# Optimization experiments

Hardware: AMD Instinct MI355X
Metric: run time of the kernel (lower is better)

## Reference

```python
import jax, jax.numpy as jnp
import numpy as np

NH = 16      # num_heads
EPS = 1e-6   # RMSNorm eps


def rmsnorm(x, w):
    return x * jax.lax.rsqrt(jnp.mean(x * x, axis=-1, keepdims=True) + EPS) * w


def rotate_half(x):
    x1, x2 = jnp.split(x, 2, axis=-1)
    return jnp.concatenate([-x2, x1], axis=-1)


def apply_rope(x, cos, sin):
    # x: [B,H,N,hd]; cos/sin: [N,hd]
    return x * cos + rotate_half(x) * sin


def attention(x, qkv_w, qkv_b, qn_w, kn_w, proj_w, proj_b, cos, sin):
    B, N, C = x.shape
    hd = C // NH
    qkv = (x @ qkv_w.T + qkv_b).reshape(B, N, 3, NH, hd).transpose(2, 0, 3, 1, 4)
    q, k, v = qkv[0], qkv[1], qkv[2]            # [B,H,N,hd]
    q = apply_rope(rmsnorm(q, qn_w), cos, sin)
    k = apply_rope(rmsnorm(k, kn_w), cos, sin)
    scores = jnp.einsum('bhqd,bhkd->bhqk', q, k) / jnp.sqrt(jnp.float32(hd))
    attn = jax.nn.softmax(scores, axis=-1)
    out = jnp.einsum('bhqk,bhkd->bhqd', attn, v)
    out = out.transpose(0, 2, 1, 3).reshape(B, N, C)
    return out @ proj_w.T + proj_b


def jit_block(x, c, cos_s, sin_s, cos_t, sin_t,
              norm1_w, norm2_w, norm3_w,
              qkv_s_w, qkv_s_b, qn_s_w, kn_s_w, proj_s_w, proj_s_b,
              qkv_t_w, qkv_t_b, qn_t_w, kn_t_w, proj_t_w, proj_t_b,
              w12_w, w12_b, w3_w, w3_b, ada_w, ada_b):
    B, T, L, D = x.shape
    mods = (jax.nn.silu(c) @ ada_w.T + ada_b).reshape(B, 9, D)
    sh_s, sc_s, g_s = mods[:, 0], mods[:, 1], mods[:, 2]
    sh_t, sc_t, g_t = mods[:, 3], mods[:, 4], mods[:, 5]
    sh_m, sc_m, g_m = mods[:, 6], mods[:, 7], mods[:, 8]

    # spatial attention over L, batched over B*T
    xs = x.reshape(B * T, L, D)
    sh = jnp.repeat(sh_s, T, axis=0)
    sc = jnp.repeat(sc_s, T, axis=0)
    g = jnp.repeat(g_s, T, axis=0)
    xs_n = rmsnorm(xs, norm1_w) * (1 + sc[:, None, :]) + sh[:, None, :]
    xs = xs + g[:, None, :] * attention(xs_n, qkv_s_w, qkv_s_b, qn_s_w, kn_s_w,
                                        proj_s_w, proj_s_b, cos_s, sin_s)
    x = xs.reshape(B, T, L, D)

    # temporal attention over T, batched over B*L
    xt = x.transpose(0, 2, 1, 3).reshape(B * L, T, D)
    sh = jnp.repeat(sh_t, L, axis=0)
    sc = jnp.repeat(sc_t, L, axis=0)
    g = jnp.repeat(g_t, L, axis=0)
    xt_n = rmsnorm(xt, norm2_w) * (1 + sc[:, None, :]) + sh[:, None, :]
    xt = xt + g[:, None, :] * attention(xt_n, qkv_t_w, qkv_t_b, qn_t_w, kn_t_w,
                                        proj_t_w, proj_t_b, cos_t, sin_t)
    x = xt.reshape(B, L, T, D).transpose(0, 2, 1, 3)

    # SwiGLU FFN with adaLN modulation + gate
    x_n = rmsnorm(x, norm3_w) * (1 + sc_m[:, None, None, :]) + sh_m[:, None, None, :]
    h12 = x_n @ w12_w.T + w12_b
    h1, h2 = jnp.split(h12, 2, axis=-1)
    mlp_out = (jax.nn.silu(h1) * h2) @ w3_w.T + w3_b
    return x + g_m[:, None, None, :] * mlp_out


def _rope_tables(n, hd):
    inv = 1.0 / (10000.0 ** (np.arange(0, hd, 2, dtype=np.float64) / hd))
    ang = np.arange(n, dtype=np.float64)[:, None] * inv[None, :]
    cos = np.concatenate([np.cos(ang), np.cos(ang)], -1).astype(np.float32)
    sin = np.concatenate([np.sin(ang), np.sin(ang)], -1).astype(np.float32)
    return jnp.asarray(cos), jnp.asarray(sin)


def setup_inputs() -> dict:
    key = jax.random.key(0)
    B, T, L, D = 2, 16, 256, 1024
    HD = D // NH
    HFF = int(int(D * 4.0) * 2 / 3)  # 2730
    ks = jax.random.split(key, 16)
    s = 0.02
    cos_s, sin_s = _rope_tables(L, HD)
    cos_t, sin_t = _rope_tables(T, HD)
    return {
        'x': jax.random.normal(ks[0], (B, T, L, D), jnp.float32),
        'c': jax.random.normal(ks[1], (B, D), jnp.float32),
        'cos_s': cos_s, 'sin_s': sin_s, 'cos_t': cos_t, 'sin_t': sin_t,
        'norm1_w': jnp.ones((D,), jnp.float32),
        'norm2_w': jnp.ones((D,), jnp.float32),
        'norm3_w': jnp.ones((D,), jnp.float32),
        'qkv_s_w': jax.random.normal(ks[2], (3 * D, D), jnp.float32) * s,
        'qkv_s_b': jnp.zeros((3 * D,), jnp.float32),
        'qn_s_w': jnp.ones((HD,), jnp.float32),
        'kn_s_w': jnp.ones((HD,), jnp.float32),
        'proj_s_w': jax.random.normal(ks[3], (D, D), jnp.float32) * s,
        'proj_s_b': jnp.zeros((D,), jnp.float32),
        'qkv_t_w': jax.random.normal(ks[4], (3 * D, D), jnp.float32) * s,
        'qkv_t_b': jnp.zeros((3 * D,), jnp.float32),
        'qn_t_w': jnp.ones((HD,), jnp.float32),
        'kn_t_w': jnp.ones((HD,), jnp.float32),
        'proj_t_w': jax.random.normal(ks[5], (D, D), jnp.float32) * s,
        'proj_t_b': jnp.zeros((D,), jnp.float32),
        'w12_w': jax.random.normal(ks[6], (2 * HFF, D), jnp.float32) * s,
        'w12_b': jnp.zeros((2 * HFF,), jnp.float32),
        'w3_w': jax.random.normal(ks[7], (D, HFF), jnp.float32) * s,
        'w3_b': jnp.zeros((D,), jnp.float32),
        'ada_w': jax.random.normal(ks[8], (9 * D, D), jnp.float32) * s,
        'ada_b': jnp.zeros((9 * D,), jnp.float32),
    }


def reference(x, c, cos_s, sin_s, cos_t, sin_t,
              norm1_w, norm2_w, norm3_w,
              qkv_s_w, qkv_s_b, qn_s_w, kn_s_w, proj_s_w, proj_s_b,
              qkv_t_w, qkv_t_b, qn_t_w, kn_t_w, proj_t_w, proj_t_b,
              w12_w, w12_b, w3_w, w3_b, ada_w, ada_b):
    return jit_block(x, c, cos_s, sin_s, cos_t, sin_t,
                     norm1_w, norm2_w, norm3_w,
                     qkv_s_w, qkv_s_b, qn_s_w, kn_s_w, proj_s_w, proj_s_b,
                     qkv_t_w, qkv_t_b, qn_t_w, kn_t_w, proj_t_w, proj_t_b,
                     w12_w, w12_b, w3_w, w3_b, ada_w, ada_b)
```

## Files before the change

### kernel.cpp

```cpp
#include <hip/hip_runtime.h>
#include <cstdint>
#include <cstddef>

typedef unsigned short u16;
typedef __attribute__((ext_vector_type(8))) short short8;
typedef __attribute__((ext_vector_type(4))) float f32x4;

__device__ __forceinline__ float bf2f(u16 u) {
  union { uint32_t u; float f; } x; x.u = ((uint32_t)u) << 16; return x.f;
}
__device__ __forceinline__ u16 f2bf(float f) {
  union { float f; uint32_t u; } x; x.f = f;
  uint32_t r = x.u + 0x7FFFu + ((x.u >> 16) & 1u);
  return (u16)(r >> 16);
}
__device__ __forceinline__ float silu_f(float x) { return x / (1.f + __expf(-x)); }

__device__ __forceinline__ void glds16(const u16* g, u16* l) {
  __builtin_amdgcn_global_load_lds(
      (const __attribute__((address_space(1))) void*)g,
      (__attribute__((address_space(3))) void*)l, 16, 0, 0);
}

#define MFMA16 __builtin_amdgcn_mfma_f32_16x16x32_bf16

__device__ __forceinline__ void wg_barrier() {
  asm volatile("" ::: "memory");
  __builtin_amdgcn_s_barrier();
  asm volatile("" ::: "memory");
}

__global__ void cvt2_kernel(const float* __restrict__ in0, u16* __restrict__ out0, int n0,
                            const float* __restrict__ in1, u16* __restrict__ out1, int n1) {
  int i = (blockIdx.x * 256 + threadIdx.x) * 4;
  const float* in; u16* out;
  if (i < n0) { in = in0 + i; out = out0 + i; }
  else { i -= n0; if (i >= n1) return; in = in1 + i; out = out1 + i; }
  float4 v = *(const float4*)in;
  ushort4 o; o.x = f2bf(v.x); o.y = f2bf(v.y); o.z = f2bf(v.z); o.w = f2bf(v.w);
  *(ushort4*)out = o;
}

__global__ void cvt3_kernel(const float* __restrict__ w12, u16* __restrict__ W1, u16* __restrict__ W2,
                            const float* __restrict__ w3, u16* __restrict__ W3) {
  int i = blockIdx.x * 256 + threadIdx.x;
  const int n1 = 2816 * 1024;
  const int n3 = 1024 * 2816;
  if (i < n1) {
    int r = i >> 10, c = i & 1023;
    W1[i] = f2bf(r < 2730 ? w12[(size_t)r * 1024 + c] : 0.f);
  } else if (i < 2 * n1) {
    int j = i - n1; int r = j >> 10, c = j & 1023;
    W2[j] = f2bf(r < 2730 ? w12[(size_t)(r + 2730) * 1024 + c] : 0.f);
  } else {
    int j = i - 2 * n1; if (j >= n3) return;
    int r = j / 2816, c = j - r * 2816;
    W3[j] = f2bf(c < 2730 ? w3[(size_t)r * 2730 + c] : 0.f);
  }
}

__global__ void mods_kernel(const float* __restrict__ c, const float* __restrict__ ada_w,
                            const float* __restrict__ ada_b, float* __restrict__ mods) {
  int j = blockIdx.x * 4 + (threadIdx.x >> 6);
  int lane = threadIdx.x & 63;
  float a0 = 0.f, a1 = 0.f;
  for (int k = lane; k < 1024; k += 64) {
    float w = ada_w[(size_t)j * 1024 + k];
    a0 += silu_f(c[k]) * w;
    a1 += silu_f(c[1024 + k]) * w;
  }
  #pragma unroll
  for (int off = 32; off > 0; off >>= 1) { a0 += __shfl_down(a0, off); a1 += __shfl_down(a1, off); }
  if (lane == 0) {
    float bb = ada_b[j];
    mods[j] = a0 + bb;
    mods[9216 + j] = a1 + bb;
  }
}

__global__ __launch_bounds__(256) void norm_mod_kernel(
    const float* __restrict__ X, u16* __restrict__ Y,
    const float* __restrict__ nw, const float* __restrict__ mods,
    int sh_idx, int transpose) {
  int row = blockIdx.x;
  int b = row >> 12;
  int in_row;
  if (transpose) { int rem = row & 4095; int l = rem >> 4, t = rem & 15; in_row = (b << 12) + (t << 8) + l; }
  else in_row = row;
  int tid = threadIdx.x;
  float4 v = ((const float4*)(X + (size_t)in_row * 1024))[tid];
  float ss = v.x * v.x + v.y * v.y + v.z * v.z + v.w * v.w;
  #pragma unroll
  for (int off = 32; off > 0; off >>= 1) ss += __shfl_down(ss, off);
  __shared__ float red[4];
  if ((tid & 63) == 0) red[tid >> 6] = ss;
  __syncthreads();
  float rms = rsqrtf((red[0] + red[1] + red[2] + red[3]) * (1.f / 1024.f) + 1e-6f);
  const float* mb = mods + (size_t)b * 9216 + (size_t)sh_idx * 1024;
  float4 sh = ((const float4*)mb)[tid];
  float4 sc = ((const float4*)(mb + 1024))[tid];
  float4 w  = ((const float4*)nw)[tid];
  ushort4 o;
  o.x = f2bf(v.x * rms * w.x * (1.f + sc.x) + sh.x);
  o.y = f2bf(v.y * rms * w.y * (1.f + sc.y) + sh.y);
  o.z = f2bf(v.z * rms * w.z * (1.f + sc.z) + sh.z);
  o.w = f2bf(v.w * rms * w.w * (1.f + sc.w) + sh.w);
  ((ushort4*)(Y + (size_t)row * 1024))[tid] = o;
}

#define CHK2(b, s) (((b) * 4 + (s)) << 13)
#define CHK3(b, s) (((b) * 3 + (s)) << 13)

__device__ __forceinline__ void stage_half(const u16* __restrict__ gp, int ldk,
                                           int row_base, int k0,
                                           u16* Sbase, int slot_u16,
                                           int wid, int srow, int scol) {
  #pragma unroll
  for (int c = 0; c < 2; c++) {
    int row = c * 64 + wid * 8 + srow;
    glds16(gp + (size_t)(row_base + row) * ldk + (k0 + scol),
           Sbase + slot_u16 + c * 4096 + wid * 512);
  }
}

template<int MODE>
__global__ __launch_bounds__(512, 2) void gemm256_n128(
    const u16* __restrict__ A, const u16* __restrict__ W,
    const float* __restrict__ bias, void* __restrict__ Cv,
    int K, int ldc,
    const float* __restrict__ base, const float* __restrict__ mods, int gidx) {
  __shared__ u16 S[49152];
  const int tid = threadIdx.x, wid = tid >> 6, lane = tid & 63;
  const int wm = wid >> 1, wn = wid & 1;
  const int quad = lane >> 4, r = lane & 15;
  const int bid = blockIdx.x, xcd = bid & 7, l = bid >> 3;
  const int mt = (xcd << 2) | (l & 3), nt = l >> 2;
  const int m0 = mt * 256, n0 = nt * 128;

  const int srow = lane >> 3;
  const int scol = ((lane & 7) ^ srow) << 3;
  const int kx0 = (quad * 8) ^ ((r & 7) << 3);
  const int kx1 = (32 + quad * 8) ^ ((r & 7) << 3);
  const int aslot = wm >> 1;
  const int arow = ((wm & 1) * 64 + r) * 64;
  const int brow = (wn * 64 + r) * 64;

  f32x4 zero = {0.f, 0.f, 0.f, 0.f};
  f32x4 acc[4][4];
  #pragma unroll
  for (int i = 0; i < 4; i++)
    #pragma unroll
    for (int j = 0; j < 4; j++) acc[i][j] = zero;
  short8 fAa[4][2], fBa[4][2], fAb[4][2], fBb[4][2];

  const int nk = K >> 6;

  const u16* gA0c0 = A + (size_t)(m0 +       wid * 8 + srow) * K + scol + 128;
  const u16* gA0c1 = A + (size_t)(m0 +  64 + wid * 8 + srow) * K + scol + 128;
  const u16* gA1c0 = A + (size_t)(m0 + 128 + wid * 8 + srow) * K + scol + 128;
  const u16* gA1c1 = A + (size_t)(m0 + 192 + wid * 8 + srow) * K + scol + 128;
  const u16* gBc0  = W + (size_t)(n0 +       wid * 8 + srow) * K + scol + 128;
  const u16* gBc1  = W + (size_t)(n0 +  64 + wid * 8 + srow) * K + scol + 128;

  stage_half(A, K, m0,       0, S, CHK3(0,0), wid, srow, scol);
  stage_half(A, K, m0 + 128, 0, S, CHK3(0,1), wid, srow, scol);
  stage_half(W, K, n0,       0, S, CHK3(0,2), wid, srow, scol);
  stage_half(A, K, m0,       64, S, CHK3(1,0), wid, srow, scol);
  stage_half(A, K, m0 + 128, 64, S, CHK3(1,1), wid, srow, scol);
  stage_half(W, K, n0,       64, S, CHK3(1,2), wid, srow, scol);
  asm volatile("s_waitcnt vmcnt(0)" ::: "memory");
  __builtin_amdgcn_s_barrier();

  {
    const u16* cA = S + CHK3(0, aslot);
    const u16* cB = S + CHK3(0, 2);
    #pragma unroll
    for (int f = 0; f < 4; f++) {
      fAa[f][0] = *(const short8*)(cA + arow + f * 1024 + kx0);
      fAa[f][1] = *(const short8*)(cA + arow + f * 1024 + kx1);
    }
    #pragma unroll
    for (int j = 0; j < 4; j++) {
      fBa[j][0] = *(const short8*)(cB + brow + j * 1024 + kx0);
      fBa[j][1] = *(const short8*)(cB + brow + j * 1024 + kx1);
    }
  }
  asm volatile("s_waitcnt lgkmcnt(0)" ::: "memory");
  __builtin_amdgcn_s_barrier();

  for (int u2 = 0; u2 < nk; u2 += 2) {
    const int s2a = (u2 + 2 < nk);
    if (s2a) {
      u16* Sb = S + wid * 512;
      glds16(gA0c0, Sb);          glds16(gA0c1, Sb + 4096);
      glds16(gA1c0, Sb + 8192);   glds16(gA1c1, Sb + 12288);
      glds16(gBc0,  Sb + 16384);  glds16(gBc1,  Sb + 20480);
      gA0c0 += 64; gA0c1 += 64; gA1c0 += 64; gA1c1 += 64; gBc0 += 64; gBc1 += 64;
    }
    {
      const u16* cA = S + CHK3(1, aslot);
      const u16* cB = S + CHK3(1, 2);
      #pragma unroll
      for (int f = 0; f < 4; f++) {
        fAb[f][0] = *(const short8*)(cA + arow + f * 1024 + kx0);
        fAb[f][1] = *(const short8*)(cA + arow + f * 1024 + kx1);
      }
      #pragma unroll
      for (int j = 0; j < 4; j++) {
        fBb[j][0] = *(const short8*)(cB + brow + j * 1024 + kx0);
        fBb[j][1] = *(const short8*)(cB + brow + j * 1024 + kx1);
      }
    }
    __builtin_amdgcn_s_setprio(1);
    #pragma unroll
    for (int f = 0; f < 4; f++)
      #pragma unroll
      for (int j = 0; j < 4; j++) {
        acc[f][j] = MFMA16(fAa[f][0], fBa[j][0], acc[f][j], 0, 0, 0);
        acc[f][j] = MFMA16(fAa[f][1], fBa[j][1], acc[f][j], 0, 0, 0);
      }
    __builtin_amdgcn_s_setprio(0);
    asm volatile("s_waitcnt lgkmcnt(0)" ::: "memory");
    if (s2a) asm volatile("s_waitcnt vmcnt(0)" ::: "memory");
    __builtin_amdgcn_s_barrier();

    const int s2b = (u2 + 3 < nk);
    if (s2b) {
      u16* Sb = S + 24576 + wid * 512;
      glds16(gA0c0, Sb);          glds16(gA0c1, Sb + 4096);
      glds16(gA1c0, Sb + 8192);   glds16(gA1c1, Sb + 12288);
      glds16(gBc0,  Sb + 16384);  glds16(gBc1,  Sb + 20480);
      gA0c0 += 64; gA0c1 += 64; gA1c0 += 64; gA1c1 += 64; gBc0 += 64; gBc1 += 64;
    }
    if (s2a) {
      const u16* cA = S + CHK3(0, aslot);
      const u16* cB = S + CHK3(0, 2);
      #pragma unroll
      for (int f = 0; f < 4; f++) {
        fAa[f][0] = *(const short8*)(cA + arow + f * 1024 + kx0);
        fAa[f][1] = *(const short8*)(cA + arow + f * 1024 + kx1);
      }
      #pragma unroll
      for (int j = 0; j < 4; j++) {
        fBa[j][0] = *(const short8*)(cB + brow + j * 1024 + kx0);
        fBa[j][1] = *(const short8*)(cB + brow + j * 1024 + kx1);
      }
    }
    __builtin_amdgcn_s_setprio(1);
    #pragma unroll
    for (int f = 0; f < 4; f++)
      #pragma unroll
      for (int j = 0; j < 4; j++) {
        acc[f][j] = MFMA16(fAb[f][0], fBb[j][0], acc[f][j], 0, 0, 0);
        acc[f][j] = MFMA16(fAb[f][1], fBb[j][1], acc[f][j], 0, 0, 0);
      }
    __builtin_amdgcn_s_setprio(0);
    if (s2a) asm volatile("s_waitcnt lgkmcnt(0)" ::: "memory");
    if (s2b) asm volatile("s_waitcnt vmcnt(0)" ::: "memory");
    __builtin_amdgcn_s_barrier();
  }

  float* Cf = (float*)Cv;
  u16* Ch = (u16*)Cv;
  #pragma unroll
  for (int f = 0; f < 4; f++) {
    int row = m0 + wm * 64 + f * 16 + quad * 4;
    #pragma unroll
    for (int j = 0; j < 4; j++) {
      int col = n0 + wn * 64 + j * 16 + r;
      float bv = bias[col];
      #pragma unroll
      for (int rr = 0; rr < 4; rr++) {
        int ri = row + rr;
        float vv = acc[f][j][rr] + bv;
        if (MODE == 0) {
          Cf[(size_t)ri * ldc + col] = vv;
        } else if (MODE == 1) {
          Ch[(size_t)ri * ldc + col] = f2bf(vv);
        } else {
          int ro = ri;
          if (MODE == 3) { int rem = ri & 4095; ro = (ri & ~4095) + ((rem & 15) << 8) + (rem >> 4); }
          int b = ri >> 12;
          float g = mods[(size_t)b * 9216 + (size_t)gidx * 1024 + col];
          Cf[(size_t)ro * 1024 + col] = base[(size_t)ro * 1024 + col] + g * vv;
        }
      }
    }
  }
}

__global__ __launch_bounds__(512, 2) void gemm256_w12(
    const u16* __restrict__ A, const u16* __restrict__ W1, const u16* __restrict__ W2,
    const float* __restrict__ bias, u16* __restrict__ Hb) {
  __shared__ u16 S[65536];
  const int tid = threadIdx.x, wid = tid >> 6, lane = tid & 63;
  const int wm = wid >> 2, wn = wid & 3;
  const int quad = lane >> 4, r = lane & 15;
  const int bid = blockIdx.x, xcd = bid & 7, l = bid >> 3;
  const int mt = (xcd << 2) | (l & 3), nt = l >> 2;
  const int m0 = mt * 256, n0 = nt * 128;

  const int srow = lane >> 3;
  const int scol = ((lane & 7) ^ srow) << 3;
  const int kx0 = (quad * 8) ^ ((r & 7) << 3);
  const int kx1 = (32 + quad * 8) ^ ((r & 7) << 3);
  const int arow = (wm * 64 + r) * 64;
  const int brow = (wn * 32 + r) * 64;
  const int K = 1024, nk = 16;

  f32x4 zero = {0.f, 0.f, 0.f, 0.f};
  f32x4 acc1[8][2], acc2[8][2];
  #pragma unroll
  for (int i = 0; i < 8; i++)
    #pragma unroll
    for (int j = 0; j < 2; j++) { acc1[i][j] = zero; acc2[i][j] = zero; }
  short8 fA[4][2], fW1[2][2], fW2[2][2];

  const u16* gA0c0 = A  + (size_t)(m0 +       wid * 8 + srow) * K + scol + 128;
  const u16* gA0c1 = A  + (size_t)(m0 +  64 + wid * 8 + srow) * K + scol + 128;
  const u16* gA1c0 = A  + (size_t)(m0 + 128 + wid * 8 + srow) * K + scol + 128;
  const u16* gA1c1 = A  + (size_t)(m0 + 192 + wid * 8 + srow) * K + scol + 128;
  const u16* gW1c0 = W1 + (size_t)(n0 +       wid * 8 + srow) * K + scol + 128;
  const u16* gW1c1 = W1 + (size_t)(n0 +  64 + wid * 8 + srow) * K + scol + 128;
  const u16* gW2c0 = W2 + (size_t)(n0 +       wid * 8 + srow) * K + scol + 128;
  const u16* gW2c1 = W2 + (size_t)(n0 +  64 + wid * 8 + srow) * K + scol + 128;

  stage_half(A,  K, m0,       0, S, CHK2(0,0), wid, srow, scol);
  stage_half(W1, K, n0,       0, S, CHK2(0,2), wid, srow, scol);
  stage_half(W2, K, n0,       0, S, CHK2(0,3), wid, srow, scol);
  stage_half(A,  K, m0 + 128, 0, S, CHK2(0,1), wid, srow, scol);
  stage_half(A,  K, m0,      64, S, CHK2(1,0), wid, srow, scol);
  stage_half(W1, K, n0,      64, S, CHK2(1,2), wid, srow, scol);
  stage_half(W2, K, n0,      64, S, CHK2(1,3), wid, srow, scol);
  stage_half(A,  K, m0 + 128,64, S, CHK2(1,1), wid, srow, scol);
  asm volatile("s_waitcnt vmcnt(8)" ::: "memory");
  __builtin_amdgcn_s_barrier();

  for (int u = 0; u < nk; ++u) {
    const int cur = u & 1;
    const int s1 = (u + 1 < nk), s2 = (u + 2 < nk);
    const u16* cA0 = S + CHK2(cur, 0);
    const u16* cA1 = S + CHK2(cur, 1);
    const u16* cW1 = S + CHK2(cur, 2);
    const u16* cW2 = S + CHK2(cur, 3);
    u16* Sb = S + cur * 32768 + wid * 512;

    #pragma unroll
    for (int f = 0; f < 4; f++) {
      fA[f][0] = *(const short8*)(cA0 + arow + f * 1024 + kx0);
      fA[f][1] = *(const short8*)(cA0 + arow + f * 1024 + kx1);
    }
    #pragma unroll
    for (int j = 0; j < 2; j++) {
      fW1[j][0] = *(const short8*)(cW1 + brow + j * 1024 + kx0);
      fW1[j][1] = *(const short8*)(cW1 + brow + j * 1024 + kx1);
      fW2[j][0] = *(const short8*)(cW2 + brow + j * 1024 + kx0);
      fW2[j][1] = *(const short8*)(cW2 + brow + j * 1024 + kx1);
    }
    wg_barrier();

    if (s2) {
      glds16(gA0c0, Sb);          glds16(gA0c1, Sb + 4096);
      glds16(gW1c0, Sb + 16384);  glds16(gW1c1, Sb + 20480);
      glds16(gW2c0, Sb + 24576);  glds16(gW2c1, Sb + 28672);
    }
    __builtin_amdgcn_s_setprio(1);
    #pragma unroll
    for (int f = 0; f < 4; f++)
      #pragma unroll
      for (int j = 0; j < 2; j++) {
        acc1[f][j] = MFMA16(fA[f][0], fW1[j][0], acc1[f][j], 0, 0, 0);
        acc1[f][j] = MFMA16(fA[f][1], fW1[j][1], acc1[f][j], 0, 0, 0);
        acc2[f][j] = MFMA16(fA[f][0], fW2[j][0], acc2[f][j], 0, 0, 0);
        acc2[f][j] = MFMA16(fA[f][1], fW2[j][1], acc2[f][j], 0, 0, 0);
      }
    __builtin_amdgcn_s_setprio(0);
    #pragma unroll
    for (int f = 0; f < 4; f++) {
      fA[f][0] = *(const short8*)(cA1 + arow + f * 1024 + kx0);
      fA[f][1] = *(const short8*)(cA1 + arow + f * 1024 + kx1);
    }
    wg_barrier();

    if (s2) { glds16(gA1c0, Sb + 8192); glds16(gA1c1, Sb + 12288); }
    gA0c0 += 64; gA0c1 += 64; gA1c0 += 64; gA1c1 += 64;
    gW1c0 += 64; gW1c1 += 64; gW2c0 += 64; gW2c1 += 64;
    __builtin_amdgcn_s_setprio(1);
    #pragma unroll
    for (int f = 0; f < 4; f++)
      #pragma unroll
      for (int j = 0; j < 2; j++) {
        acc1[4 + f][j] = MFMA16(fA[f][0], fW1[j][0], acc1[4 + f][j], 0, 0, 0);
        acc1[4 + f][j] = MFMA16(fA[f][1], fW1[j][1], acc1[4 + f][j], 0, 0, 0);
        acc2[4 + f][j] = MFMA16(fA[f][0], fW2[j][0], acc2[4 + f][j], 0, 0, 0);
        acc2[4 + f][j] = MFMA16(fA[f][1], fW2[j][1], acc2[4 + f][j], 0, 0, 0);
      }
    __builtin_amdgcn_s_setprio(0);
    if (s2)      asm volatile("s_waitcnt vmcnt(8)" ::: "memory");
    else if (s1) asm volatile("s_waitcnt vmcnt(0)" ::: "memory");
    wg_barrier();
  }

  #pragma unroll
  for (int f = 0; f < 8; f++) {
    int row = m0 + (f >> 2) * 128 + wm * 64 + (f & 3) * 16 + quad * 4;
    #pragma unroll
    for (int j = 0; j < 2; j++) {
      int col = n0 + wn * 32 + j * 16 + r;
      float b1 = (col < 2730) ? bias[col] : 0.f;
      float b2 = (col < 2730) ? bias[2730 + col] : 0.f;
      #pragma unroll
      for (int rr = 0; rr < 4; rr++) {
        float h1 = acc1[f][j][rr] + b1;
        float h2 = acc2[f][j][rr] + b2;
        Hb[(size_t)(row + rr) * 2816 + col] = f2bf(silu_f(h1) * h2);
      }
    }
  }
}

#define KSS 72
#define VSS 264
#define PSS 40
__global__ __launch_bounds__(512) void attn_s_mfma(
    const u16* __restrict__ QKV,
    const float* __restrict__ qn_w, const float* __restrict__ kn_w,
    const float* __restrict__ cosT, const float* __restrict__ sinT,
    u16* __restrict__ AO) {
  __shared__ u16 Ks[256 * KSS];
  __shared__ u16 Vt[64 * VSS];
  __shared__ u16 Pl[8 * 32 * PSS];
  int pair = blockIdx.x;
  int s = pair >> 4, h = pair & 15;
  int tid = threadIdx.x, wid = tid >> 6, lane = tid & 63;
  int quad = lane >> 4, r = lane & 15;

  if (tid < 256) {
    int j = tid;
    size_t rowb = ((size_t)(s * 256 + j)) * 3072 + (size_t)h * 64;
    const short8* kr = (const short8*)(QKV + rowb + 1024);
    float xk[64]; float ssq = 0.f;
    #pragma unroll
    for (int cg = 0; cg < 8; cg++) {
      short8 kk = kr[cg];
      #pragma unroll
      for (int e = 0; e < 8; e++) { float v = bf2f((u16)kk[e]); xk[cg * 8 + e] = v; ssq += v * v; }
    }
    float rms = rsqrtf(ssq * (1.f / 64.f) + 1e-6f);
    short8 kq[8];
    #pragma unroll
    for (int d = 0; d < 32; d++) {
      float a = xk[d] * rms * kn_w[d];
      float b2 = xk[d + 32] * rms * kn_w[d + 32];
      u16 o0 = f2bf(a * cosT[j * 64 + d] - b2 * sinT[j * 64 + d]);
      u16 o1 = f2bf(b2 * cosT[j * 64 + 32 + d] + a * sinT[j * 64 + 32 + d]);
      kq[d >> 3][d & 7] = (short)o0;
      kq[(d + 32) >> 3][d & 7] = (short)o1;
    }
    #pragma unroll
    for (int cg = 0; cg < 8; cg++) *(short8*)(Ks + j * KSS + cg * 8) = kq[cg];
  } else {
    int j = tid - 256;
    size_t rowb = ((size_t)(s * 256 + j)) * 3072 + (size_t)h * 64;
    const short8* vr = (const short8*)(QKV + rowb + 2048);
    #pragma unroll
    for (int cg = 0; cg < 8; cg++) {
      short8 vv = vr[cg];
      #pragma unroll
      for (int e = 0; e < 8; e++) Vt[(cg * 8 + e) * VSS + j] = (u16)vv[e];
    }
  }

  int qbase = wid * 32;
  short8 qa[2][2];
  float lrow[2][4];
  {
    float qv[2][2][8];
    float ssq[2] = {0.f, 0.f};
    #pragma unroll
    for (int i = 0; i < 2; i++) {
      int grow = s * 256 + qbase + i * 16 + r;
      #pragma unroll
      for (int kk = 0; kk < 2; kk++) {
        short8 qraw = *(const short8*)(QKV + (size_t)grow * 3072 + h * 64 + kk * 32 + quad * 8);
        #pragma unroll
        for (int e = 0; e < 8; e++) { float v = bf2f((u16)qraw[e]); qv[i][kk][e] = v; ssq[i] += v * v; }
      }
    }
    #pragma unroll
    for (int i = 0; i < 2; i++) {
      float sv = ssq[i];
      sv += __shfl_xor(sv, 16);
      sv += __shfl_xor(sv, 32);
      float rms = rsqrtf(sv * (1.f / 64.f) + 1e-6f);
      int qrow = qbase + i * 16 + r;
      #pragma unroll
      for (int e = 0; e < 8; e++) {
        int d0 = quad * 8 + e;
        float a = qv[i][0][e] * rms * qn_w[d0];
        float b2 = qv[i][1][e] * rms * qn_w[d0 + 32];
        qa[i][0][e] = (short)f2bf(a * cosT[qrow * 64 + d0] - b2 * sinT[qrow * 64 + d0]);
        qa[i][1][e] = (short)f2bf(b2 * cosT[qrow * 64 + 32 + d0] + a * sinT[qrow * 64 + 32 + d0]);
      }
    }
  }
  __syncthreads();

  f32x4 zero = {0.f, 0.f, 0.f, 0.f};
  f32x4 acc[2][16];
  #pragma unroll
  for (int i = 0; i < 2; i++)
    #pragma unroll
    for (int j = 0; j < 16; j++) acc[i][j] = zero;
  #pragma unroll
  for (int kk = 0; kk < 2; kk++) {
    #pragma unroll
    for (int j = 0; j < 16; j++) {
      short8 bfr = *(const short8*)(Ks + (j * 16 + r) * KSS + kk * 32 + quad * 8);
      acc[0][j] = MFMA16(qa[0][kk], bfr, acc[0][j], 0, 0, 0);
      acc[1][j] = MFMA16(qa[1][kk], bfr, acc[1][j], 0, 0, 0);
    }
  }

  #pragma unroll
  for (int i = 0; i < 2; i++) {
    #pragma unroll
    for (int rr = 0; rr < 4; rr++) {
      float mx = acc[i][0][rr];
      #pragma unroll
      for (int j = 1; j < 16; j++) mx = fmaxf(mx, acc[i][j][rr]);
      #pragma unroll
      for (int msk = 1; msk < 16; msk <<= 1) mx = fmaxf(mx, __shfl_xor(mx, msk));
      float ls = 0.f;
      #pragma unroll
      for (int j = 0; j < 16; j++) { float p = __expf((acc[i][j][rr] - mx) * 0.125f); acc[i][j][rr] = p; ls += p; }
      #pragma unroll
      for (int msk = 1; msk < 16; msk <<= 1) ls += __shfl_xor(ls, msk);
      lrow[i][rr] = ls;
    }
  }

  f32x4 oacc[2][4];
  #pragma unroll
  for (int i = 0; i < 2; i++)
    #pragma unroll
    for (int j = 0; j < 4; j++) oacc[i][j] = zero;
  u16* plw = Pl + wid * 32 * PSS;
  #pragma unroll
  for (int kk = 0; kk < 8; kk++) {
    #pragma unroll
    for (int i = 0; i < 2; i++)
      #pragma unroll
      for (int jj = 0; jj < 2; jj++) {
        int j = kk * 2 + jj;
        #pragma unroll
        for (int rr = 0; rr < 4; rr++)
          plw[(i * 16 + quad * 4 + rr) * PSS + jj * 16 + r] = f2bf(acc[i][j][rr]);
      }
    short8 pa0 = *(const short8*)(plw + r * PSS + quad * 8);
    short8 pa1 = *(const short8*)(plw + (16 + r) * PSS + quad * 8);
    #pragma unroll
    for (int j4 = 0; j4 < 4; j4++) {
      short8 vfr = *(const short8*)(Vt + (j4 * 16 + r) * VSS + kk * 32 + quad * 8);
      oacc[0][j4] = MFMA16(pa0, vfr, oacc[0][j4], 0, 0, 0);
      oacc[1][j4] = MFMA16(pa1, vfr, oacc[1][j4], 0, 0, 0);
    }
  }

  #pragma unroll
  for (int i = 0; i < 2; i++) {
    #pragma unroll
    for (int rr = 0; rr < 4; rr++) {
      float inv = 1.f / lrow[i][rr];
      int row = s * 256 + qbase + i * 16 + quad * 4 + rr;
      #pragma unroll
      for (int j4 = 0; j4 < 4; j4++)
        AO[(size_t)row * 1024 + h * 64 + j4 * 16 + r] = f2bf(oacc[i][j4][rr] * inv);
    }
  }
}

__global__ __launch_bounds__(256) void attn_t_kernel(
    const u16* __restrict__ QKV,
    const float* __restrict__ qn_w, const float* __restrict__ kn_w,
    const float* __restrict__ cosT, const float* __restrict__ sinT,
    u16* __restrict__ AO) {
  __shared__ u16 kb[256 * 64];
  __shared__ u16 vb[256 * 64];
  int bl = blockIdx.x;
  int tid = threadIdx.x;
  int h = tid >> 4, t = tid & 15;
  size_t rowbase = ((size_t)(bl * 16 + t)) * 3072;
  int slot = h * 16 + t;
  {
    const u16* kr = QKV + rowbase + 1024 + h * 64;
    float xk[64]; float ss = 0.f;
    #pragma unroll
    for (int d = 0; d < 64; d++) { xk[d] = bf2f(kr[d]); ss += xk[d] * xk[d]; }
    float rms = rsqrtf(ss * (1.f / 64.f) + 1e-6f);
    #pragma unroll
    for (int d = 0; d < 64; d++) xk[d] *= rms * kn_w[d];
    #pragma unroll
    for (int d = 0; d < 32; d++) {
      float a = xk[d], bb = xk[d + 32];
      kb[slot * 64 + d]      = f2bf(a * cosT[t * 64 + d]       - bb * sinT[t * 64 + d]);
      kb[slot * 64 + 32 + d] = f2bf(bb * cosT[t * 64 + 32 + d] + a * sinT[t * 64 + 32 + d]);
    }
    const u16* vr = QKV + rowbase + 2048 + h * 64;
    #pragma unroll
    for (int d = 0; d < 64; d++) vb[slot * 64 + d] = vr[d];
  }
  float q[64];
  {
    const u16* qr = QKV + rowbase + h * 64;
    float ss = 0.f;
    #pragma unroll
    for (int d = 0; d < 64; d++) { q[d] = bf2f(qr[d]); ss += q[d] * q[d]; }
    float rms = rsqrtf(ss * (1.f / 64.f) + 1e-6f);
    #pragma unroll
    for (int d = 0; d < 64; d++) q[d] *= rms * qn_w[d];
    #pragma unroll
    for (int d = 0; d < 32; d++) {
      float a = q[d], bb = q[d + 32];
      q[d]      = a * cosT[t * 64 + d]       - bb * sinT[t * 64 + d];
      q[d + 32] = bb * cosT[t * 64 + 32 + d] + a * sinT[t * 64 + 32 + d];
    }
  }
  __syncthreads();
  float scv[16]; float mx = -1e30f;
  #pragma unroll
  for (int j = 0; j < 16; j++) {
    float sc = 0.f;
    const short8* krow = (const short8*)(kb + (h * 16 + j) * 64);
    #pragma unroll
    for (int vv = 0; vv < 8; vv++) {
      short8 kk = krow[vv];
      #pragma unroll
      for (int e = 0; e < 8; e++) sc += q[vv * 8 + e] * bf2f((u16)kk[e]);
    }
    scv[j] = sc * 0.125f;
    mx = fmaxf(mx, scv[j]);
  }
  float ssum = 0.f;
  #pragma unroll
  for (int j = 0; j < 16; j++) { scv[j] = __expf(scv[j] - mx); ssum += scv[j]; }
  float inv = 1.f / ssum;
  float o[64];
  #pragma unroll
  for (int d = 0; d < 64; d++) o[d] = 0.f;
  #pragma unroll
  for (int j = 0; j < 16; j++) {
    const short8* vrow = (const short8*)(vb + (h * 16 + j) * 64);
    #pragma unroll
    for (int vv = 0; vv < 8; vv++) {
      short8 vk = vrow[vv];
      #pragma unroll
      for (int e = 0; e < 8; e++) o[vv * 8 + e] += scv[j] * bf2f((u16)vk[e]);
    }
  }
  u16* op = AO + ((size_t)(bl * 16 + t)) * 1024 + h * 64;
  #pragma unroll
  for (int d = 0; d < 64; d++) op[d] = f2bf(o[d] * inv);
}

extern "C" void kernel_launch(void* const* d_in, const int* in_sizes, int n_in,
                              void* d_out, int out_size, void* d_ws, size_t ws_size,
                              hipStream_t stream) {
  const float* x        = (const float*)d_in[0];
  const float* c        = (const float*)d_in[1];
  const float* cos_s    = (const float*)d_in[2];
  const float* sin_s    = (const float*)d_in[3];
  const float* cos_t    = (const float*)d_in[4];
  const float* sin_t    = (const float*)d_in[5];
  const float* norm1w   = (const float*)d_in[6];
  const float* norm2w   = (const float*)d_in[7];
  const float* norm3w   = (const float*)d_in[8];
  const float* qkv_s_w  = (const float*)d_in[9];
  const float* qkv_s_b  = (const float*)d_in[10];
  const float* qn_s_w   = (const float*)d_in[11];
  const float* kn_s_w   = (const float*)d_in[12];
  const float* proj_s_w = (const float*)d_in[13];
  const float* proj_s_b = (const float*)d_in[14];
  const float* qkv_t_w  = (const float*)d_in[15];
  const float* qkv_t_b  = (const float*)d_in[16];
  const float* qn_t_w   = (const float*)d_in[17];
  const float* kn_t_w   = (const float*)d_in[18];
  const float* proj_t_w = (const float*)d_in[19];
  const float* proj_t_b = (const float*)d_in[20];
  const float* w12_w    = (const float*)d_in[21];
  const float* w12_b    = (const float*)d_in[22];
  const float* w3_w     = (const float*)d_in[23];
  const float* w3_b     = (const float*)d_in[24];
  const float* ada_w    = (const float*)d_in[25];
  const float* ada_b    = (const float*)d_in[26];
  float* out = (float*)d_out;

  char* wsp = (char*)d_ws;
  size_t off = 0;
  auto alloc = [&](size_t bytes) { size_t p = off; off += (bytes + 255) & ~(size_t)255; return p; };
  float* modsb = (float*)(wsp + alloc(2 * 9216 * 4));
  u16*   BIG   = (u16*)  (wsp + alloc((size_t)8192 * 3072 * 2));
  char*  XnP   = (char*) (wsp + alloc((size_t)8192 * 1024 * 4));
  u16*   AO    = (u16*)  (wsp + alloc((size_t)8192 * 1024 * 2));
  u16*   Wq    = (u16*)  (wsp + alloc((size_t)3072 * 1024 * 2));
  u16*   Wp    = (u16*)  (wsp + alloc((size_t)2816 * 1024 * 2));
  u16*   W3b   = (u16*)  (wsp + alloc((size_t)1024 * 2816 * 2));
  u16* W1p = Wq;
  u16* W2p = Wp;
  u16* Xn  = (u16*)XnP;
  float* Xcur = out;

  dim3 blk(256);
  dim3 blk512(512);
  mods_kernel<<<2304, blk, 0, stream>>>(c, ada_w, ada_b, modsb);

  {
    int n0 = 3072 * 1024, n1 = 1024 * 1024;
    cvt2_kernel<<<(n0 + n1) / 1024, blk, 0, stream>>>(qkv_s_w, Wq, n0, proj_s_w, Wp, n1);
  }
  norm_mod_kernel<<<8192, blk, 0, stream>>>(x, Xn, norm1w, modsb, 0, 0);
  gemm256_n128<1><<<dim3(32 * 24), blk512, 0, stream>>>(Xn, Wq, qkv_s_b, BIG, 1024, 3072, nullptr, nullptr, 0);
  attn_s_mfma<<<dim3(512), blk512, 0, stream>>>(BIG, qn_s_w, kn_s_w, cos_s, sin_s, AO);
  gemm256_n128<2><<<dim3(32 * 8), blk512, 0, stream>>>(AO, Wp, proj_s_b, Xcur, 1024, 1024, x, modsb, 2);

  {
    int n0 = 3072 * 1024, n1 = 1024 * 1024;
    cvt2_kernel<<<(n0 + n1) / 1024, blk, 0, stream>>>(qkv_t_w, Wq, n0, proj_t_w, Wp, n1);
  }
  norm_mod_kernel<<<8192, blk, 0, stream>>>(Xcur, Xn, norm2w, modsb, 3, 1);
  gemm256_n128<1><<<dim3(32 * 24), blk512, 0, stream>>>(Xn, Wq, qkv_t_b, BIG, 1024, 3072, nullptr, nullptr, 0);
  attn_t_kernel<<<512, blk, 0, stream>>>(BIG, qn_t_w, kn_t_w, cos_t, sin_t, AO);
  gemm256_n128<3><<<dim3(32 * 8), blk512, 0, stream>>>(AO, Wp, proj_t_b, Xcur, 1024, 1024, Xcur, modsb, 5);

  {
    int tot = 2 * 2816 * 1024 + 1024 * 2816;
    cvt3_kernel<<<(tot + 255) / 256, blk, 0, stream>>>(w12_w, W1p, W2p, w3_w, W3b);
  }
  norm_mod_kernel<<<8192, blk, 0, stream>>>(Xcur, Xn, norm3w, modsb, 6, 0);
  gemm256_w12<<<dim3(32 * 22), blk512, 0, stream>>>(Xn, W1p, W2p, w12_b, BIG);
  gemm256_n128<2><<<dim3(32 * 8), blk512, 0, stream>>>(BIG, W3b, w3_b, out, 2816, 1024, Xcur, modsb, 8);
}
```

Before: 641.3 us.

## Shrink SwiGLU GEMM M-tile to 128 with register-prefetched LDS double buffer

The fused W1/W2 SwiGLU GEMM now uses 128x128 output tiles instead of 256x128, doubling the grid to 1408 blocks and halving the accumulator registers and shared memory. The main loop is restructured into a two-stage ping-pong. Fragments for the next K-step are read from LDS into a second register set while MFMAs run on the current set, and global-to-LDS loads are issued one step ahead. This aims to improve occupancy, tail balance and latency hiding, at the cost of lower operand reuse per block and full vmcnt(0) waits each step.

```diff
diff --git a/kernel.cpp b/kernel.cpp
--- a/kernel.cpp
+++ b/kernel.cpp
@@ -108,7 +108,6 @@
   ((ushort4*)(Y + (size_t)row * 1024))[tid] = o;
 }
 
-#define CHK2(b, s) (((b) * 4 + (s)) << 13)
 #define CHK3(b, s) (((b) * 3 + (s)) << 13)
 
 __device__ __forceinline__ void stage_half(const u16* __restrict__ gp, int ldk,
@@ -289,16 +288,16 @@
   }
 }
 
-__global__ __launch_bounds__(512, 2) void gemm256_w12(
+__global__ __launch_bounds__(512, 2) void gemm128_w12(
     const u16* __restrict__ A, const u16* __restrict__ W1, const u16* __restrict__ W2,
     const float* __restrict__ bias, u16* __restrict__ Hb) {
-  __shared__ u16 S[65536];
+  __shared__ u16 S[49152];
   const int tid = threadIdx.x, wid = tid >> 6, lane = tid & 63;
   const int wm = wid >> 2, wn = wid & 3;
   const int quad = lane >> 4, r = lane & 15;
   const int bid = blockIdx.x, xcd = bid & 7, l = bid >> 3;
-  const int mt = (xcd << 2) | (l & 3), nt = l >> 2;
-  const int m0 = mt * 256, n0 = nt * 128;
+  const int mt = (xcd << 3) | (l & 7), nt = l >> 3;
+  const int m0 = mt * 128, n0 = nt * 128;
 
   const int srow = lane >> 3;
   const int scol = ((lane & 7) ^ srow) << 3;
@@ -309,101 +308,135 @@
   const int K = 1024, nk = 16;
 
   f32x4 zero = {0.f, 0.f, 0.f, 0.f};
-  f32x4 acc1[8][2], acc2[8][2];
-  #pragma unroll
-  for (int i = 0; i < 8; i++)
+  f32x4 acc1[4][2], acc2[4][2];
+  #pragma unroll
+  for (int i = 0; i < 4; i++)
     #pragma unroll
     for (int j = 0; j < 2; j++) { acc1[i][j] = zero; acc2[i][j] = zero; }
-  short8 fA[4][2], fW1[2][2], fW2[2][2];
-
-  const u16* gA0c0 = A  + (size_t)(m0 +       wid * 8 + srow) * K + scol + 128;
-  const u16* gA0c1 = A  + (size_t)(m0 +  64 + wid * 8 + srow) * K + scol + 128;
-  const u16* gA1c0 = A  + (size_t)(m0 + 128 + wid * 8 + srow) * K + scol + 128;
-  const u16* gA1c1 = A  + (size_t)(m0 + 192 + wid * 8 + srow) * K + scol + 128;
-  const u16* gW1c0 = W1 + (size_t)(n0 +       wid * 8 + srow) * K + scol + 128;
-  const u16* gW1c1 = W1 + (size_t)(n0 +  64 + wid * 8 + srow) * K + scol + 128;
-  const u16* gW2c0 = W2 + (size_t)(n0 +       wid * 8 + srow) * K + scol + 128;
-  const u16* gW2c1 = W2 + (size_t)(n0 +  64 + wid * 8 + srow) * K + scol + 128;
-
-  stage_half(A,  K, m0,       0, S, CHK2(0,0), wid, srow, scol);
-  stage_half(W1, K, n0,       0, S, CHK2(0,2), wid, srow, scol);
-  stage_half(W2, K, n0,       0, S, CHK2(0,3), wid, srow, scol);
-  stage_half(A,  K, m0 + 128, 0, S, CHK2(0,1), wid, srow, scol);
-  stage_half(A,  K, m0,      64, S, CHK2(1,0), wid, srow, scol);
-  stage_half(W1, K, n0,      64, S, CHK2(1,2), wid, srow, scol);
-  stage_half(W2, K, n0,      64, S, CHK2(1,3), wid, srow, scol);
-  stage_half(A,  K, m0 + 128,64, S, CHK2(1,1), wid, srow, scol);
-  asm volatile("s_waitcnt vmcnt(8)" ::: "memory");
+  short8 fAa[4][2], fW1a[2][2], fW2a[2][2];
+  short8 fAb[4][2], fW1b[2][2], fW2b[2][2];
+
+  const u16* gAc0  = A  + (size_t)(m0 +      wid * 8 + srow) * K + scol + 128;
+  const u16* gAc1  = A  + (size_t)(m0 + 64 + wid * 8 + srow) * K + scol + 128;
+  const u16* gW1c0 = W1 + (size_t)(n0 +      wid * 8 + srow) * K + scol + 128;
+  const u16* gW1c1 = W1 + (size_t)(n0 + 64 + wid * 8 + srow) * K + scol + 128;
+  const u16* gW2c0 = W2 + (size_t)(n0 +      wid * 8 + srow) * K + scol + 128;
+  const u16* gW2c1 = W2 + (size_t)(n0 + 64 + wid * 8 + srow) * K + scol + 128;
+
+  stage_half(A,  K, m0, 0, S, 0,     wid, srow, scol);
+  stage_half(W1, K, n0, 0, S, 8192,  wid, srow, scol);
+  stage_half(W2, K, n0, 0, S, 16384, wid, srow, scol);
+  stage_half(A,  K, m0, 64, S, 24576 + 0,     wid, srow, scol);
+  stage_half(W1, K, n0, 64, S, 24576 + 8192,  wid, srow, scol);
+  stage_half(W2, K, n0, 64, S, 24576 + 16384, wid, srow, scol);
+  asm volatile("s_waitcnt vmcnt(0)" ::: "memory");
   __builtin_amdgcn_s_barrier();
 
-  for (int u = 0; u < nk; ++u) {
-    const int cur = u & 1;
-    const int s1 = (u + 1 < nk), s2 = (u + 2 < nk);
-    const u16* cA0 = S + CHK2(cur, 0);
-    const u16* cA1 = S + CHK2(cur, 1);
-    const u16* cW1 = S + CHK2(cur, 2);
-    const u16* cW2 = S + CHK2(cur, 3);
-    u16* Sb = S + cur * 32768 + wid * 512;
-
+  {
+    const u16* cA  = S;
+    const u16* cW1 = S + 8192;
+    const u16* cW2 = S + 16384;
     #pragma unroll
     for (int f = 0; f < 4; f++) {
-      fA[f][0] = *(const short8*)(cA0 + arow + f * 1024 + kx0);
-      fA[f][1] = *(const short8*)(cA0 + arow + f * 1024 + kx1);
+      fAa[f][0] = *(const short8*)(cA + arow + f * 1024 + kx0);
+      fAa[f][1] = *(const short8*)(cA + arow + f * 1024 + kx1);
     }
     #pragma unroll
     for (int j = 0; j < 2; j++) {
-      fW1[j][0] = *(const short8*)(cW1 + brow + j * 1024 + kx0);
-      fW1[j][1] = *(const short8*)(cW1 + brow + j * 1024 + kx1);
-      fW2[j][0] = *(const short8*)(cW2 + brow + j * 1024 + kx0);
-      fW2[j][1] = *(const short8*)(cW2 + brow + j * 1024 + kx1);
-    }
-    wg_barrier();
-
-    if (s2) {
-      glds16(gA0c0, Sb);          glds16(gA0c1, Sb + 4096);
-      glds16(gW1c0, Sb + 16384);  glds16(gW1c1, Sb + 20480);
-      glds16(gW2c0, Sb + 24576);  glds16(gW2c1, Sb + 28672);
+      fW1a[j][0] = *(const short8*)(cW1 + brow + j * 1024 + kx0);
+      fW1a[j][1] = *(const short8*)(cW1 + brow + j * 1024 + kx1);
+      fW2a[j][0] = *(const short8*)(cW2 + brow + j * 1024 + kx0);
+      fW2a[j][1] = *(const short8*)(cW2 + brow + j * 1024 + kx1);
+    }
+  }
+  asm volatile("s_waitcnt lgkmcnt(0)" ::: "memory");
+  __builtin_amdgcn_s_barrier();
+
+  for (int u2 = 0; u2 < nk; u2 += 2) {
+    const int s2a = (u2 + 2 < nk);
+    if (s2a) {
+      u16* Sb = S + wid * 512;
+      glds16(gAc0,  Sb);          glds16(gAc1,  Sb + 4096);
+      glds16(gW1c0, Sb + 8192);   glds16(gW1c1, Sb + 12288);
+      glds16(gW2c0, Sb + 16384);  glds16(gW2c1, Sb + 20480);
+      gAc0 += 64; gAc1 += 64; gW1c0 += 64; gW1c1 += 64; gW2c0 += 64; gW2c1 += 64;
+    }
+    {
+      const u16* cA  = S + 24576;
+      const u16* cW1 = S + 24576 + 8192;
+      const u16* cW2 = S + 24576 + 16384;
+      #pragma unroll
+      for (int f = 0; f < 4; f++) {
+        fAb[f][0] = *(const short8*)(cA + arow + f * 1024 + kx0);
+        fAb[f][1] = *(const short8*)(cA + arow + f * 1024 + kx1);
+      }
+      #pragma unroll
+      for (int j = 0; j < 2; j++) {
+        fW1b[j][0] = *(const short8*)(cW1 + brow + j * 1024 + kx0);
+        fW1b[j][1] = *(const short8*)(cW1 + brow + j * 1024 + kx1);
+        fW2b[j][0] = *(const short8*)(cW2 + brow + j * 1024 + kx0);
+        fW2b[j][1] = *(const short8*)(cW2 + brow + j * 1024 + kx1);
+      }
     }
     __builtin_amdgcn_s_setprio(1);
     #pragma unroll
     for (int f = 0; f < 4; f++)
       #pragma unroll
       for (int j = 0; j < 2; j++) {
-        acc1[f][j] = MFMA16(fA[f][0], fW1[j][0], acc1[f][j], 0, 0, 0);
-        acc1[f][j] = MFMA16(fA[f][1], fW1[j][1], acc1[f][j], 0, 0, 0);
-        acc2[f][j] = MFMA16(fA[f][0], fW2[j][0], acc2[f][j], 0, 0, 0);
-        acc2[f][j] = MFMA16(fA[f][1], fW2[j][1], acc2[f][j], 0, 0, 0);
+        acc1[f][j] = MFMA16(fAa[f][0], fW1a[j][0], acc1[f][j], 0, 0, 0);
+        acc1[f][j] = MFMA16(fAa[f][1], fW1a[j][1], acc1[f][j], 0, 0, 0);
+        acc2[f][j] = MFMA16(fAa[f][0], fW2a[j][0], acc2[f][j], 0, 0, 0);
+        acc2[f][j] = MFMA16(fAa[f][1], fW2a[j][1], acc2[f][j], 0, 0, 0);
       }
     __builtin_amdgcn_s_setprio(0);
-    #pragma unroll
-    for (int f = 0; f < 4; f++) {
-      fA[f][0] = *(const short8*)(cA1 + arow + f * 1024 + kx0);
-      fA[f][1] = *(const short8*)(cA1 + arow + f * 1024 + kx1);
-    }
-    wg_barrier();
-
-    if (s2) { glds16(gA1c0, Sb + 8192); glds16(gA1c1, Sb + 12288); }
-    gA0c0 += 64; gA0c1 += 64; gA1c0 += 64; gA1c1 += 64;
-    gW1c0 += 64; gW1c1 += 64; gW2c0 += 64; gW2c1 += 64;
+    asm volatile("s_waitcnt lgkmcnt(0)" ::: "memory");
+    if (s2a) asm volatile("s_waitcnt vmcnt(0)" ::: "memory");
+    __builtin_amdgcn_s_barrier();
+
+    const int s2b = (u2 + 3 < nk);
+    if (s2b) {
+      u16* Sb = S + 24576 + wid * 512;
+      glds16(gAc0,  Sb);          glds16(gAc1,  Sb + 4096);
+      glds16(gW1c0, Sb + 8192);   glds16(gW1c1, Sb + 12288);
+      glds16(gW2c0, Sb + 16384);  glds16(gW2c1, Sb + 20480);
+      gAc0 += 64; gAc1 += 64; gW1c0 += 64; gW1c1 += 64; gW2c0 += 64; gW2c1 += 64;
+    }
+    if (s2a) {
+      const u16* cA  = S;
+      const u16* cW1 = S + 8192;
+      const u16* cW2 = S + 16384;
+      #pragma unroll
+      for (int f = 0; f < 4; f++) {
+        fAa[f][0] = *(const short8*)(cA + arow + f * 1024 + kx0);
+        fAa[f][1] = *(const short8*)(cA + arow + f * 1024 + kx1);
+      }
+      #pragma unroll
+      for (int j = 0; j < 2; j++) {
+        fW1a[j][0] = *(const short8*)(cW1 + brow + j * 1024 + kx0);
+        fW1a[j][1] = *(const short8*)(cW1 + brow + j * 1024 + kx1);
+        fW2a[j][0] = *(const short8*)(cW2 + brow + j * 1024 + kx0);
+        fW2a[j][1] = *(const short8*)(cW2 + brow + j * 1024 + kx1);
+      }
+    }
     __builtin_amdgcn_s_setprio(1);
     #pragma unroll
     for (int f = 0; f < 4; f++)
       #pragma unroll
       for (int j = 0; j < 2; j++) {
-        acc1[4 + f][j] = MFMA16(fA[f][0], fW1[j][0], acc1[4 + f][j], 0, 0, 0);
-        acc1[4 + f][j] = MFMA16(fA[f][1], fW1[j][1], acc1[4 + f][j], 0, 0, 0);
-        acc2[4 + f][j] = MFMA16(fA[f][0], fW2[j][0], acc2[4 + f][j], 0, 0, 0);
-        acc2[4 + f][j] = MFMA16(fA[f][1], fW2[j][1], acc2[4 + f][j], 0, 0, 0);
+        acc1[f][j] = MFMA16(fAb[f][0], fW1b[j][0], acc1[f][j], 0, 0, 0);
+        acc1[f][j] = MFMA16(fAb[f][1], fW1b[j][1], acc1[f][j], 0, 0, 0);
+        acc2[f][j] = MFMA16(fAb[f][0], fW2b[j][0], acc2[f][j], 0, 0, 0);
+        acc2[f][j] = MFMA16(fAb[f][1], fW2b[j][1], acc2[f][j], 0, 0, 0);
       }
     __builtin_amdgcn_s_setprio(0);
-    if (s2)      asm volatile("s_waitcnt vmcnt(8)" ::: "memory");
-    else if (s1) asm volatile("s_waitcnt vmcnt(0)" ::: "memory");
-    wg_barrier();
-  }
-
-  #pragma unroll
-  for (int f = 0; f < 8; f++) {
-    int row = m0 + (f >> 2) * 128 + wm * 64 + (f & 3) * 16 + quad * 4;
+    if (s2a) asm volatile("s_waitcnt lgkmcnt(0)" ::: "memory");
+    if (s2b) asm volatile("s_waitcnt vmcnt(0)" ::: "memory");
+    __builtin_amdgcn_s_barrier();
+  }
+
+  #pragma unroll
+  for (int f = 0; f < 4; f++) {
+    int row = m0 + wm * 64 + f * 16 + quad * 4;
     #pragma unroll
     for (int j = 0; j < 2; j++) {
       int col = n0 + wn * 32 + j * 16 + r;
@@ -737,6 +770,6 @@
     cvt3_kernel<<<(tot + 255) / 256, blk, 0, stream>>>(w12_w, W1p, W2p, w3_w, W3b);
   }
   norm_mod_kernel<<<8192, blk, 0, stream>>>(Xcur, Xn, norm3w, modsb, 6, 0);
-  gemm256_w12<<<dim3(32 * 22), blk512, 0, stream>>>(Xn, W1p, W2p, w12_b, BIG);
+  gemm128_w12<<<dim3(1408), blk512, 0, stream>>>(Xn, W1p, W2p, w12_b, BIG);
   gemm256_n128<2><<<dim3(32 * 8), blk512, 0, stream>>>(BIG, W3b, w3_b, out, 2816, 1024, Xcur, modsb, 8);
 }
```

New measurement: 663.9 us. 3.5% more time.
